# Optimization experiments

Hardware: AMD Instinct MI355X
Metric: run time of the kernel (lower is better)

The kernel has to match this reference:

```python
import jax, jax.numpy as jnp
import numpy as np
import math

HIDDEN, HEADS, D_K = 768, 12, 64
BS, SEQ = 4, 2048


def setup_inputs() -> dict:
    key = jax.random.key(0)
    ks = jax.random.split(key, 5)
    s = 1.0 / math.sqrt(HIDDEN)
    return {
        "x": jax.random.normal(ks[0], (BS, SEQ, HIDDEN), dtype=jnp.float32),
        "Wq": jax.random.normal(ks[1], (HIDDEN, HIDDEN), dtype=jnp.float32) * s,
        "bq": jnp.zeros((HIDDEN,), jnp.float32),
        "Wk": jax.random.normal(ks[2], (HIDDEN, HIDDEN), dtype=jnp.float32) * s,
        "bk": jnp.zeros((HIDDEN,), jnp.float32),
        "Wv": jax.random.normal(ks[3], (HIDDEN, HIDDEN), dtype=jnp.float32) * s,
        "bv": jnp.zeros((HIDDEN,), jnp.float32),
        "Wo": jax.random.normal(ks[4], (HIDDEN, HIDDEN), dtype=jnp.float32) * s,
        "bo": jnp.zeros((HIDDEN,), jnp.float32),
    }


def reference(x, Wq, bq, Wk, bk, Wv, bv, Wo, bo):
    bs, seq, _ = x.shape
    # projections; nn.Linear computes x @ W.T + b
    def proj(W, b):
        y = jnp.einsum("bsd,ed->bse", x, W) + b
        return y.reshape(bs, seq, HEADS, D_K).transpose(0, 2, 1, 3)  # [b,h,s,d]
    q, k, v = proj(Wq, bq), proj(Wk, bk), proj(Wv, bv)
    scores = jnp.einsum("bhqd,bhkd->bhqk", q, k) / jnp.sqrt(jnp.float32(D_K))
    attn = jax.nn.softmax(scores, axis=-1)  # dropout = 0 (eval)
    ctx = jnp.einsum("bhqk,bhkd->bhqd", attn, v)
    ctx = ctx.transpose(0, 2, 1, 3).reshape(bs, seq, HIDDEN)
    return jnp.einsum("bsd,ed->bse", ctx, Wo) + bo
```

## Files before the change

### kernel.cpp

```cpp
#include <hip/hip_runtime.h>
#include <hip/hip_bf16.h>

#define HID 768
#define NHEAD 12
#define DKH 64
#define BSZ 4
#define SEQ 2048
#define MTOT (BSZ*SEQ)
#define NBH (BSZ*NHEAD)

typedef __attribute__((ext_vector_type(8))) short   s16x8;
typedef __attribute__((ext_vector_type(8))) __bf16  bf16x8;
typedef __attribute__((ext_vector_type(4))) __bf16  bf16x4;
typedef __attribute__((ext_vector_type(4))) float   f32x4;

#define MFMA16x32(A,B,C) __builtin_amdgcn_mfma_f32_16x16x32_bf16((A),(B),(C),0,0,0)

__device__ __forceinline__ unsigned short f2bf(float f) {
  union { float f; unsigned int u; } a; a.f = f;
  return (unsigned short)((a.u + 0x7FFFu + ((a.u >> 16) & 1u)) >> 16);
}

__device__ __forceinline__ void gload_lds16(const unsigned short* g, unsigned short* l) {
  __builtin_amdgcn_global_load_lds((const __attribute__((address_space(1))) void*)g,
                                   (__attribute__((address_space(3))) void*)l, 16, 0, 0);
}

__global__ __launch_bounds__(256) void cvtall_kernel(const float* __restrict__ x,
                                                     const float* __restrict__ w0,
                                                     const float* __restrict__ w1,
                                                     const float* __restrict__ w2,
                                                     const float* __restrict__ w3,
                                                     unsigned short* __restrict__ xb,
                                                     unsigned short* __restrict__ wb) {
  const int bid = blockIdx.x;
  const float* src; unsigned short* dst; int off;
  if (bid < 6144) {
    src = x; dst = xb; off = bid * 1024;
  } else {
    const int t = bid - 6144;
    const int wi = t / 576;
    const int ro = t - wi * 576;
    src = (wi == 0) ? w0 : (wi == 1) ? w1 : (wi == 2) ? w2 : w3;
    dst = wb + (size_t)wi * HID * HID;
    off = ro * 1024;
  }
  const int i = off + threadIdx.x * 4;
  float4 v = *(const float4*)(src + i);
  ushort4 o;
  o.x = f2bf(v.x); o.y = f2bf(v.y); o.z = f2bf(v.z); o.w = f2bf(v.w);
  *(ushort4*)(dst + i) = o;
}

#define VM4 asm volatile("s_waitcnt vmcnt(4)" ::: "memory")
#define VM0 asm volatile("s_waitcnt vmcnt(0)" ::: "memory")
#define CFENCE asm volatile("" ::: "memory")

#define G0_STAGE(BUF, KTN)                                                  \
    _Pragma("unroll")                                                       \
    for (int i = 0; i < 2; ++i) {                                           \
      const int c = wave * 2 + i;                                           \
      gload_lds16(Aptr + (size_t)(c*16 + sr4) * HID + (KTN) + sc4,          \
                  As[BUF] + c*512);                                         \
      gload_lds16(Wptr + (size_t)(c*16 + sr4) * HID + (KTN) + sc4,          \
                  Bs[BUF] + c*512);                                         \
    }

#define G0_COMPUTE(BUF)                                                     \
    {                                                                       \
      const char* ab = (const char*)As[BUF];                                \
      const char* bb = (const char*)Bs[BUF];                                \
      bf16x8 af[4], bfr[4];                                                 \
      _Pragma("unroll")                                                     \
      for (int mb = 0; mb < 4; ++mb) {                                      \
        const int r = wm + mb*16 + l16;                                     \
        af[mb] = *(const bf16x8*)(ab + r*64 + (((lg) ^ (r & 3)) << 4));     \
      }                                                                     \
      _Pragma("unroll")                                                     \
      for (int nb = 0; nb < 4; ++nb) {                                      \
        const int r = wn + nb*16 + l16;                                     \
        bfr[nb] = *(const bf16x8*)(bb + r*64 + (((lg) ^ (r & 3)) << 4));    \
      }                                                                     \
      _Pragma("unroll")                                                     \
      for (int mb = 0; mb < 4; ++mb)                                        \
        _Pragma("unroll")                                                   \
        for (int nb = 0; nb < 4; ++nb)                                      \
          acc[mb][nb] = MFMA16x32(af[mb], bfr[nb], acc[mb][nb]);            \
    }

#define G0_STEP(BUF, KTN, PF)                                               \
  {                                                                         \
    if (PF) { G0_STAGE(((BUF)+2)%3, KTN) }                                  \
    G0_COMPUTE(BUF)                                                         \
    if (PF) { VM4; } else { VM0; }                                          \
    __builtin_amdgcn_sched_barrier(0);                                      \
    __builtin_amdgcn_s_barrier();                                           \
    CFENCE;                                                                 \
  }

__global__ __launch_bounds__(256, 3) void gemm0_kernel(
    const unsigned short* __restrict__ A,
    const unsigned short* __restrict__ W,
    const float* __restrict__ bias0,
    const float* __restrict__ bias1,
    const float* __restrict__ bias2,
    unsigned short* __restrict__ out,
    unsigned short* __restrict__ vtimg)
{
  __shared__ unsigned short As[3][128*32];
  __shared__ unsigned short Bs[3][128*32];
  const int tid  = threadIdx.x;
  const int wave = tid >> 6, lane = tid & 63;
  const int l16  = lane & 15, lg = lane >> 4;
  const int f    = blockIdx.x;
  const int xcd  = f & 7, rr = f >> 3;
  const int bx   = xcd*8 + (rr & 7), by = rr >> 3;
  const int m0   = bx * 128, n0 = by * 128;
  const int wm   = (wave & 1) * 64,  wn = (wave >> 1) * 64;

  const f32x4 z4 = {0.f, 0.f, 0.f, 0.f};
  f32x4 acc[4][4];
#pragma unroll
  for (int i = 0; i < 4; ++i)
#pragma unroll
    for (int j = 0; j < 4; ++j) acc[i][j] = z4;

  const int sr4 = lane >> 2;
  const int sc4 = ((lane & 3) ^ (sr4 & 3)) << 3;
  const unsigned short* Aptr = A + (size_t)m0 * HID;
  const unsigned short* Wptr = W + (size_t)n0 * HID;

  G0_STAGE(0, 0)
  G0_STAGE(1, 32)
  VM4;
  __builtin_amdgcn_sched_barrier(0);
  __builtin_amdgcn_s_barrier();
  CFENCE;

#pragma unroll 1
  for (int tt = 0; tt < 7; ++tt) {
    G0_STEP(0, (tt*3+2)*32, 1)
    G0_STEP(1, (tt*3+3)*32, 1)
    G0_STEP(2, (tt*3+4)*32, 1)
  }
  G0_STEP(0, 23*32, 1)
  G0_STEP(1, 0, 0)
  G0_COMPUTE(2)

  const float QSCALE = 0.18033688011112042f;
  const int which = (n0 + wn) / HID;
  if (which == 2) {
    const int h = (n0 + wn - 2*HID) >> 6;
#pragma unroll
    for (int nb = 0; nb < 4; ++nb) {
      const int d = nb*16 + l16;
      const float bias = bias2[h*64 + d];
#pragma unroll
      for (int mb = 0; mb < 4; ++mb) {
        const int m    = m0 + wm + mb*16 + lg*4;
        const int b    = m >> 11, s = m & (SEQ - 1);
        const int tile = s >> 6;
        const int slot = ((s & 63) >> 2) ^ l16;
        ushort4 w;
        w.x = f2bf(acc[mb][nb][0] + bias);
        w.y = f2bf(acc[mb][nb][1] + bias);
        w.z = f2bf(acc[mb][nb][2] + bias);
        w.w = f2bf(acc[mb][nb][3] + bias);
        *(ushort4*)(vtimg + ((((size_t)(b*NHEAD + h)*32 + tile)*64 + d)*64 + slot*4)) = w;
      }
    }
  } else {
    const float* bp  = (which == 0) ? bias0 : bias1;
    const float scl  = (which == 0) ? QSCALE : 1.0f;
    const int e_base = n0 + wn - which*HID;
#pragma unroll
    for (int nb = 0; nb < 4; ++nb) {
      const int e = e_base + nb*16 + l16;
      const float bias = bp[e];
      const int h = e >> 6, d = e & 63;
#pragma unroll
      for (int mb = 0; mb < 4; ++mb)
#pragma unroll
        for (int j = 0; j < 4; ++j) {
          const int m = m0 + wm + mb*16 + lg*4 + j;
          const int b = m >> 11, s = m & (SEQ - 1);
          const float v = (acc[mb][nb][j] + bias) * scl;
          out[((((size_t)which*BSZ + b)*NHEAD + h)*SEQ + s)*DKH + d] = f2bf(v);
        }
    }
  }
}

#define GEMM_STEP(CUR, KTN, DOPREF)                                         \
  {                                                                         \
    if (DOPREF) {                                                           \
      _Pragma("unroll")                                                     \
      for (int i = 0; i < 4; ++i) {                                         \
        const int c = wave * 4 + i;                                         \
        gload_lds16(Aptr + (size_t)(c*8 + sr) * HID + (KTN) + sc8,          \
                    As[(CUR)^1] + c*512);                                   \
      }                                                                     \
      _Pragma("unroll")                                                     \
      for (int i = 0; i < 2; ++i) {                                         \
        const int c = wave * 2 + i;                                         \
        gload_lds16(Wptr + (size_t)(c*8 + sr) * HID + (KTN) + sc8,          \
                    Bs[(CUR)^1] + c*512);                                   \
      }                                                                     \
    }                                                                       \
    const char* ab = (const char*)As[CUR];                                  \
    const char* bb = (const char*)Bs[CUR];                                  \
    _Pragma("unroll")                                                       \
    for (int kk = 0; kk < 2; ++kk) {                                        \
      bf16x8 af[4], bfr[2];                                                 \
      _Pragma("unroll")                                                     \
      for (int mb = 0; mb < 4; ++mb) {                                      \
        const int r = wm + mb*16 + l16;                                     \
        af[mb] = *(const bf16x8*)(ab + r*128 + (((kk*4 + lg) ^ (l16 & 7)) << 4)); \
      }                                                                     \
      _Pragma("unroll")                                                     \
      for (int nb = 0; nb < 2; ++nb) {                                      \
        const int r = wn + nb*16 + l16;                                     \
        bfr[nb] = *(const bf16x8*)(bb + r*128 + (((kk*4 + lg) ^ (l16 & 7)) << 4)); \
      }                                                                     \
      _Pragma("unroll")                                                     \
      for (int mb = 0; mb < 4; ++mb)                                        \
        _Pragma("unroll")                                                   \
        for (int nb = 0; nb < 2; ++nb)                                      \
          acc[mb][nb] = MFMA16x32(af[mb], bfr[nb], acc[mb][nb]);            \
    }                                                                       \
    __syncthreads();                                                        \
  }

__global__ __launch_bounds__(256) void gemm1_kernel(
    const unsigned short* __restrict__ A,
    const unsigned short* __restrict__ W,
    const float* __restrict__ bias0,
    float* __restrict__ out)
{
  __shared__ unsigned short As[2][128*64];
  __shared__ unsigned short Bs[2][64*64];
  const int tid  = threadIdx.x;
  const int wave = tid >> 6, lane = tid & 63;
  const int l16  = lane & 15, lg = lane >> 4;
  const int f    = blockIdx.x;
  const int xcd  = f & 7, rr = f >> 3;
  const int bx   = xcd*8 + (rr & 7), by = rr >> 3;
  const int m0   = bx * 128, n0 = by * 64;
  const int wm   = (wave & 1) * 64,  wn = (wave >> 1) * 32;

  const f32x4 z4 = {0.f, 0.f, 0.f, 0.f};
  f32x4 acc[4][2];
#pragma unroll
  for (int i = 0; i < 4; ++i)
#pragma unroll
    for (int j = 0; j < 2; ++j) acc[i][j] = z4;

  const int sr  = lane >> 3;
  const int sc8 = ((lane & 7) ^ sr) << 3;
  const unsigned short* Aptr = A + (size_t)m0 * HID;
  const unsigned short* Wptr = W + (size_t)n0 * HID;

#pragma unroll
  for (int i = 0; i < 4; ++i) {
    const int c = wave * 4 + i;
    gload_lds16(Aptr + (size_t)(c*8 + sr) * HID + sc8, As[0] + c*512);
  }
#pragma unroll
  for (int i = 0; i < 2; ++i) {
    const int c = wave * 2 + i;
    gload_lds16(Wptr + (size_t)(c*8 + sr) * HID + sc8, Bs[0] + c*512);
  }
  __syncthreads();

#pragma unroll 1
  for (int tt = 0; tt < 6; ++tt) {
    GEMM_STEP(0, (2*tt+1)*64, true)
    GEMM_STEP(1, (2*tt+2)*64, (tt < 5))
  }

#pragma unroll
  for (int nb = 0; nb < 2; ++nb) {
    const int n = n0 + wn + nb*16 + l16;
    const float bias = bias0[n];
#pragma unroll
    for (int mb = 0; mb < 4; ++mb)
#pragma unroll
      for (int j = 0; j < 4; ++j) {
        const int m = m0 + wm + mb*16 + lg*4 + j;
        out[(size_t)m*HID + n] = acc[mb][nb][j] + bias;
      }
  }
}

#define ATTN_STEP(CUR, DOPREF)                                              \
  {                                                                         \
    if (DOPREF) {                                                           \
      gload_lds16(kSrc0, Ks[(CUR)^1] + wave*1024);                          \
      gload_lds16(kSrc1, Ks[(CUR)^1] + wave*1024 + 512);                    \
      gload_lds16(vSrc0, Vs[(CUR)^1] + wave*1024);                          \
      gload_lds16(vSrc1, Vs[(CUR)^1] + wave*1024 + 512);                    \
      kSrc0 += 64*DKH; kSrc1 += 64*DKH; vSrc0 += 4096; vSrc1 += 4096;       \
    }                                                                       \
    const char* kb = (const char*)Ks[CUR];                                  \
    const char* vb = (const char*)Vs[CUR];                                  \
    f32x4 sc[2][4];                                                         \
    __builtin_amdgcn_s_setprio(1);                                          \
    _Pragma("unroll")                                                       \
    for (int nb = 0; nb < 4; ++nb) {                                        \
      bf16x8 kf0 = *(const bf16x8*)(kb + kbase0 + nb*2048);                 \
      bf16x8 kf1 = *(const bf16x8*)(kb + kbase1 + nb*2048);                 \
      f32x4 z0 = z4, z1 = z4;                                               \
      z0 = MFMA16x32(kf0, qf[0][0], z0);                                    \
      z0 = MFMA16x32(kf1, qf[0][1], z0);                                    \
      z1 = MFMA16x32(kf0, qf[1][0], z1);                                    \
      z1 = MFMA16x32(kf1, qf[1][1], z1);                                    \
      sc[0][nb] = z0; sc[1][nb] = z1;                                       \
    }                                                                       \
    __builtin_amdgcn_s_setprio(0);                                          \
    bf16x8 pa[2][2];                                                        \
    _Pragma("unroll")                                                       \
    for (int qa = 0; qa < 2; ++qa)                                          \
      _Pragma("unroll")                                                     \
      for (int nb = 0; nb < 4; ++nb)                                        \
        _Pragma("unroll")                                                   \
        for (int j = 0; j < 4; ++j)                                         \
          pa[qa][nb>>1][(nb&1)*4 + j] =                                     \
            (__bf16)__builtin_amdgcn_exp2f(sc[qa][nb][j]);                  \
    __builtin_amdgcn_s_setprio(1);                                          \
    csum[0] = MFMA16x32(pa[0][0], ones, csum[0]);                           \
    csum[0] = MFMA16x32(pa[0][1], ones, csum[0]);                           \
    csum[1] = MFMA16x32(pa[1][0], ones, csum[1]);                           \
    csum[1] = MFMA16x32(pa[1][1], ones, csum[1]);                           \
    _Pragma("unroll")                                                       \
    for (int db = 0; db < 4; ++db) {                                        \
      bf16x4 v00 = *(const bf16x4*)(vb + vbase0 + db*2048);                 \
      bf16x4 v01 = *(const bf16x4*)(vb + vbase1 + db*2048);                 \
      bf16x4 v10 = *(const bf16x4*)(vb + vbase2 + db*2048);                 \
      bf16x4 v11 = *(const bf16x4*)(vb + vbase3 + db*2048);                 \
      bf16x8 vf0 = __builtin_shufflevector(v00, v01, 0,1,2,3,4,5,6,7);      \
      bf16x8 vf1 = __builtin_shufflevector(v10, v11, 0,1,2,3,4,5,6,7);      \
      cacc[0][db] = MFMA16x32(pa[0][0], vf0, cacc[0][db]);                  \
      cacc[0][db] = MFMA16x32(pa[0][1], vf1, cacc[0][db]);                  \
      cacc[1][db] = MFMA16x32(pa[1][0], vf0, cacc[1][db]);                  \
      cacc[1][db] = MFMA16x32(pa[1][1], vf1, cacc[1][db]);                  \
    }                                                                       \
    __builtin_amdgcn_s_setprio(0);                                          \
    __syncthreads();                                                        \
  }

__global__ __launch_bounds__(256, 3) void attn_kernel(const unsigned short* __restrict__ qkv,
                                                      const unsigned short* __restrict__ vtimg,
                                                      unsigned short* __restrict__ ctx)
{
  __shared__ unsigned short Ks[2][64*64];
  __shared__ unsigned short Vs[2][64*64];
  const int tid  = threadIdx.x;
  const int wave = tid >> 6, lane = tid & 63;
  const int l16  = lane & 15, lg = lane >> 4;
  const int f   = blockIdx.x;
  const int xcd = f & 7, idx = f >> 3;
  const int bh  = xcd * 6 + (idx >> 4);
  const int qt  = idx & 15;
  const int b   = bh / NHEAD, h = bh - b * NHEAD;
  const int q0  = qt * 128 + wave * 32;

  const unsigned short* Qg = qkv + (size_t)bh * (SEQ*DKH);
  const unsigned short* Kg = qkv + (size_t)(NBH + bh) * (SEQ*DKH);

  const int srow  = lane >> 3;
  const int scolK = ((lane & 7) ^ srow) << 3;
  const unsigned short* kSrc0 = Kg + (size_t)(wave*16 + srow) * DKH + scolK;
  const unsigned short* kSrc1 = Kg + (size_t)(wave*16 + 8 + srow) * DKH + scolK;
  const unsigned short* vSrc0 = vtimg + ((size_t)bh*32*64 + wave*16 + srow) * 64 + (lane & 7) * 8;
  const unsigned short* vSrc1 = vSrc0 + 8*64;

  const int kbase0 = l16*128 + ((lg ^ (l16 & 7)) << 4);
  const int kbase1 = l16*128 + (((lg + 4) ^ (l16 & 7)) << 4);
  const int vbase0 = l16*128 + (((lg     ) ^ l16) << 3);
  const int vbase1 = l16*128 + (((lg +  4) ^ l16) << 3);
  const int vbase2 = l16*128 + (((lg +  8) ^ l16) << 3);
  const int vbase3 = l16*128 + (((lg + 12) ^ l16) << 3);

  bf16x8 qf[2][2];
#pragma unroll
  for (int qa = 0; qa < 2; ++qa) {
    qf[qa][0] = *(const bf16x8*)(Qg + (size_t)(q0 + qa*16 + l16)*DKH + lg*8);
    qf[qa][1] = *(const bf16x8*)(Qg + (size_t)(q0 + qa*16 + l16)*DKH + 32 + lg*8);
  }

  bf16x8 ones;
#pragma unroll
  for (int e = 0; e < 8; ++e) ones[e] = (__bf16)1.0f;

  const f32x4 z4 = {0.f,0.f,0.f,0.f};
  f32x4 cacc[2][4];
  f32x4 csum[2] = {z4, z4};
#pragma unroll
  for (int qa = 0; qa < 2; ++qa)
#pragma unroll
    for (int db = 0; db < 4; ++db) cacc[qa][db] = z4;

  gload_lds16(kSrc0, Ks[0] + wave*1024);
  gload_lds16(kSrc1, Ks[0] + wave*1024 + 512);
  gload_lds16(vSrc0, Vs[0] + wave*1024);
  gload_lds16(vSrc1, Vs[0] + wave*1024 + 512);
  kSrc0 += 64*DKH; kSrc1 += 64*DKH; vSrc0 += 4096; vSrc1 += 4096;
  __syncthreads();

#pragma unroll 1
  for (int tt = 0; tt < 16; ++tt) {
    ATTN_STEP(0, true)
    ATTN_STEP(1, (tt < 15))
  }

#pragma unroll
  for (int qa = 0; qa < 2; ++qa) {
    f32x4 inv;
#pragma unroll
    for (int j = 0; j < 4; ++j) inv[j] = 1.0f / csum[qa][j];
#pragma unroll
    for (int db = 0; db < 4; ++db)
#pragma unroll
      for (int j = 0; j < 4; ++j) {
        const int srow2 = q0 + qa*16 + lg*4 + j;
        ctx[((size_t)(b*SEQ + srow2))*HID + h*DKH + db*16 + l16] = f2bf(cacc[qa][db][j] * inv[j]);
      }
  }
}

extern "C" void kernel_launch(void* const* d_in, const int* in_sizes, int n_in,
                              void* d_out, int out_size, void* d_ws, size_t ws_size,
                              hipStream_t stream) {
  (void)in_sizes; (void)n_in; (void)out_size; (void)ws_size;
  const float* x  = (const float*)d_in[0];
  const float* Wq = (const float*)d_in[1];
  const float* bq = (const float*)d_in[2];
  const float* Wk = (const float*)d_in[3];
  const float* bk = (const float*)d_in[4];
  const float* Wv = (const float*)d_in[5];
  const float* bv = (const float*)d_in[6];
  const float* Wo = (const float*)d_in[7];
  const float* bo = (const float*)d_in[8];

  unsigned short* ws   = (unsigned short*)d_ws;
  unsigned short* Xb   = ws;
  unsigned short* Wqkv = Xb + (size_t)MTOT * HID;
  unsigned short* Wob  = Wqkv + (size_t)3 * HID * HID;
  unsigned short* qkvb = Wob + (size_t)HID * HID;
  unsigned short* vtb  = qkvb + (size_t)2 * NBH * SEQ * DKH;
  unsigned short* ctxb = Xb;

  cvtall_kernel<<<6144 + 4*576, 256, 0, stream>>>(x, Wq, Wk, Wv, Wo, Xb, Wqkv);

  gemm0_kernel<<<1152, 256, 0, stream>>>(Xb, Wqkv, bq, bk, bv, qkvb, vtb);
  attn_kernel<<<768, 256, 0, stream>>>(qkvb, vtb, ctxb);
  gemm1_kernel<<<768, 256, 0, stream>>>(ctxb, Wob, bo, (float*)d_out);
}
```

Measured before the change: 126.1 us.

## Load V tiles directly from global into registers, bypassing LDS

The V operand for the PV MFMAs is now loaded straight from global memory into per-lane registers, double-buffered across iterations, instead of being staged through LDS with global_load_lds. The projection epilogue drops the XOR swizzle on the V-transposed image so each lane's global reads are contiguous. This removes half the LDS traffic and footprint per block, but adds 32 extra VGPRs of V buffers and exposes global-load latency directly to the MFMA chain. Each wave now loads the full V tile itself rather than sharing one copy across the block.

Result: slower. 264.3 us (+109.6%).

```diff
diff --git a/kernel.cpp b/kernel.cpp
--- a/kernel.cpp
+++ b/kernel.cpp
@@ -160,7 +160,7 @@
         const int m    = m0 + wm + mb*16 + lg*4;
         const int b    = m >> 11, s = m & (SEQ - 1);
         const int tile = s >> 6;
-        const int slot = ((s & 63) >> 2) ^ l16;
+        const int slot = (s & 63) >> 2;
         ushort4 w;
         w.x = f2bf(acc[mb][nb][0] + bias);
         w.y = f2bf(acc[mb][nb][1] + bias);
@@ -292,17 +292,25 @@
   }
 }
 
-#define ATTN_STEP(CUR, DOPREF)                                              \
+#define VLOAD(VS, VP)                                                       \
+    _Pragma("unroll")                                                       \
+    for (int db = 0; db < 4; ++db) {                                        \
+      VS[db][0] = *(const bf16x4*)((VP) + db*1024);                         \
+      VS[db][1] = *(const bf16x4*)((VP) + db*1024 + 16);                    \
+      VS[db][2] = *(const bf16x4*)((VP) + db*1024 + 32);                    \
+      VS[db][3] = *(const bf16x4*)((VP) + db*1024 + 48);                    \
+    }
+
+#define ATTN_STEP(CUR, VCUR, VNXT, DOPREF)                                  \
   {                                                                         \
     if (DOPREF) {                                                           \
+      VLOAD(VNXT, vPtr)                                                     \
+      vPtr += 4096;                                                         \
       gload_lds16(kSrc0, Ks[(CUR)^1] + wave*1024);                          \
       gload_lds16(kSrc1, Ks[(CUR)^1] + wave*1024 + 512);                    \
-      gload_lds16(vSrc0, Vs[(CUR)^1] + wave*1024);                          \
-      gload_lds16(vSrc1, Vs[(CUR)^1] + wave*1024 + 512);                    \
-      kSrc0 += 64*DKH; kSrc1 += 64*DKH; vSrc0 += 4096; vSrc1 += 4096;       \
+      kSrc0 += 64*DKH; kSrc1 += 64*DKH;                                     \
     }                                                                       \
     const char* kb = (const char*)Ks[CUR];                                  \
-    const char* vb = (const char*)Vs[CUR];                                  \
     f32x4 sc[2][4];                                                         \
     __builtin_amdgcn_s_setprio(1);                                          \
     _Pragma("unroll")                                                       \
@@ -333,12 +341,10 @@
     csum[1] = MFMA16x32(pa[1][1], ones, csum[1]);                           \
     _Pragma("unroll")                                                       \
     for (int db = 0; db < 4; ++db) {                                        \
-      bf16x4 v00 = *(const bf16x4*)(vb + vbase0 + db*2048);                 \
-      bf16x4 v01 = *(const bf16x4*)(vb + vbase1 + db*2048);                 \
-      bf16x4 v10 = *(const bf16x4*)(vb + vbase2 + db*2048);                 \
-      bf16x4 v11 = *(const bf16x4*)(vb + vbase3 + db*2048);                 \
-      bf16x8 vf0 = __builtin_shufflevector(v00, v01, 0,1,2,3,4,5,6,7);      \
-      bf16x8 vf1 = __builtin_shufflevector(v10, v11, 0,1,2,3,4,5,6,7);      \
+      bf16x8 vf0 = __builtin_shufflevector(VCUR[db][0], VCUR[db][1],        \
+                                           0,1,2,3,4,5,6,7);                \
+      bf16x8 vf1 = __builtin_shufflevector(VCUR[db][2], VCUR[db][3],        \
+                                           0,1,2,3,4,5,6,7);                \
       cacc[0][db] = MFMA16x32(pa[0][0], vf0, cacc[0][db]);                  \
       cacc[0][db] = MFMA16x32(pa[0][1], vf1, cacc[0][db]);                  \
       cacc[1][db] = MFMA16x32(pa[1][0], vf0, cacc[1][db]);                  \
@@ -353,7 +359,6 @@
                                                       unsigned short* __restrict__ ctx)
 {
   __shared__ unsigned short Ks[2][64*64];
-  __shared__ unsigned short Vs[2][64*64];
   const int tid  = threadIdx.x;
   const int wave = tid >> 6, lane = tid & 63;
   const int l16  = lane & 15, lg = lane >> 4;
@@ -371,15 +376,11 @@
   const int scolK = ((lane & 7) ^ srow) << 3;
   const unsigned short* kSrc0 = Kg + (size_t)(wave*16 + srow) * DKH + scolK;
   const unsigned short* kSrc1 = Kg + (size_t)(wave*16 + 8 + srow) * DKH + scolK;
-  const unsigned short* vSrc0 = vtimg + ((size_t)bh*32*64 + wave*16 + srow) * 64 + (lane & 7) * 8;
-  const unsigned short* vSrc1 = vSrc0 + 8*64;
+
+  const unsigned short* vPtr = vtimg + (size_t)bh*32*4096 + l16*64 + lg*4;
 
   const int kbase0 = l16*128 + ((lg ^ (l16 & 7)) << 4);
   const int kbase1 = l16*128 + (((lg + 4) ^ (l16 & 7)) << 4);
-  const int vbase0 = l16*128 + (((lg     ) ^ l16) << 3);
-  const int vbase1 = l16*128 + (((lg +  4) ^ l16) << 3);
-  const int vbase2 = l16*128 + (((lg +  8) ^ l16) << 3);
-  const int vbase3 = l16*128 + (((lg + 12) ^ l16) << 3);
 
   bf16x8 qf[2][2];
 #pragma unroll
@@ -400,17 +401,19 @@
 #pragma unroll
     for (int db = 0; db < 4; ++db) cacc[qa][db] = z4;
 
+  bf16x4 va[4][4], vb[4][4];
+
+  VLOAD(va, vPtr)
+  vPtr += 4096;
   gload_lds16(kSrc0, Ks[0] + wave*1024);
   gload_lds16(kSrc1, Ks[0] + wave*1024 + 512);
-  gload_lds16(vSrc0, Vs[0] + wave*1024);
-  gload_lds16(vSrc1, Vs[0] + wave*1024 + 512);
-  kSrc0 += 64*DKH; kSrc1 += 64*DKH; vSrc0 += 4096; vSrc1 += 4096;
+  kSrc0 += 64*DKH; kSrc1 += 64*DKH;
   __syncthreads();
 
 #pragma unroll 1
   for (int tt = 0; tt < 16; ++tt) {
-    ATTN_STEP(0, true)
-    ATTN_STEP(1, (tt < 15))
+    ATTN_STEP(0, va, vb, true)
+    ATTN_STEP(1, vb, va, (tt < 15))
   }
 
 #pragma unroll
```
